# Kernel optimization log

Measured on AMD Instinct MI355X. Metric: run time of the kernel, lower is better.

The kernel has to match this reference:

```python
import jax, jax.numpy as jnp
import numpy as np

WEIGHT = 0.1
SELF_WEIGHT = 1.0
OTHER_WEIGHT = 1.0

def setup_inputs() -> dict:
    key = jax.random.key(0)
    k1, k2 = jax.random.split(key)
    B, D = 8192, 128
    output = jax.random.normal(k1, (B, D), dtype=jnp.float32)
    target = jax.random.normal(k2, (B, D), dtype=jnp.float32)
    return {"output": output, "target": target}

def reference(output, target):
    # Pairwise Euclidean distances d[i, n] = ||output[i] - target[n]||_2
    # no [B, B, D] intermediate).
    B = output.shape[0]
    xx = jnp.sum(output * output, axis=-1)          # [B]
    yy = jnp.sum(target * target, axis=-1)          # [B]
    d2 = xx[:, None] + yy[None, :] - 2.0 * (output @ target.T)  # [B, B]
    d = jnp.sqrt(jnp.maximum(d2, 0.0))
    diag_sum = jnp.trace(d)                          # sum of self distances
    total_sum = jnp.sum(d)
    other_sum = total_sum - diag_sum
    loss = (-diag_sum * SELF_WEIGHT + other_sum * OTHER_WEIGHT) / B * WEIGHT
    return loss
```

## Files before the change

kernel.cpp:

```cpp
#include <hip/hip_runtime.h>
#include <stdint.h>

typedef float f32x16 __attribute__((ext_vector_type(16)));
typedef int v8i __attribute__((ext_vector_type(8)));

#define BDIM 8192

__global__ __launch_bounds__(256) void prep_kernel(const float* __restrict__ out_f,
                                                   const float* __restrict__ tgt_f,
                                                   uint8_t* __restrict__ ak,
                                                   float* __restrict__ xxyy) {
    const float* src = blockIdx.y ? tgt_f : out_f;
    uint8_t* dst = ak + (size_t)blockIdx.y * (1u << 20);
    float* nrm = xxyy + (size_t)blockIdx.y * BDIM;

    const int tid = threadIdx.x;
    const int lane = tid & 63;
    const int w = tid >> 6;
    const int jg = lane & 15;
    const int r = blockIdx.x * 16 + w * 4 + (lane >> 4);

    const float4* s4 = (const float4*)(src + (size_t)r * 128 + jg * 8);
    float4 a = s4[0], b = s4[1];

    uint32_t w0 = __builtin_amdgcn_cvt_pk_fp8_f32(a.x, a.y, 0, false);
    w0 = __builtin_amdgcn_cvt_pk_fp8_f32(a.z, a.w, w0, true);
    uint32_t w1 = __builtin_amdgcn_cvt_pk_fp8_f32(b.x, b.y, 0, false);
    w1 = __builtin_amdgcn_cvt_pk_fp8_f32(b.z, b.w, w1, true);

    *(uint2*)(dst + (jg >> 3) * 524288 + ((jg >> 2) & 1) * 262144
                  + r * 32 + (jg & 3) * 8) = make_uint2(w0, w1);

    float sq = a.x*a.x + a.y*a.y + a.z*a.z + a.w*a.w
             + b.x*b.x + b.y*b.y + b.z*b.z + b.w*b.w;
    sq += __shfl_xor(sq, 1); sq += __shfl_xor(sq, 2);
    sq += __shfl_xor(sq, 4); sq += __shfl_xor(sq, 8);
    if (jg == 0) nrm[r] = sq;
}

__global__ __launch_bounds__(256, 4) void dist_kernel(const uint8_t* __restrict__ Ak,
                                                      const uint8_t* __restrict__ Bk,
                                                      const float* __restrict__ xxg,
                                                      const float* __restrict__ yyg,
                                                      float* __restrict__ partials) {
    __shared__ float xxl[128];
    __shared__ float yyl[128];
    __shared__ float wsum[4];

    const int tid = threadIdx.x;
    const int lane = tid & 63;
    const int wid = tid >> 6;
    const int wr = wid >> 1, wc = wid & 1;
    const int bx = blockIdx.x, by = blockIdx.y;

    if (tid < 128) xxl[tid] = xxg[bx * 128 + tid];
    else           yyl[tid - 128] = yyg[by * 128 + (tid - 128)];
    __syncthreads();

    const int lm = lane & 31;
    const int fh = lane >> 5;
    const uint8_t* pa = Ak + fh * 262144 + (size_t)(bx * 128 + wr * 64 + lm) * 32;
    const uint8_t* pb = Bk + fh * 262144 + (size_t)(by * 128 + wc * 64 + lm) * 32;

    f32x16 acc[2][2] = {};
    #pragma unroll
    for (int S = 0; S < 2; ++S) {
        v8i a0 = *(const v8i*)(pa + S * 524288);
        v8i a1 = *(const v8i*)(pa + S * 524288 + 1024);
        v8i b0 = *(const v8i*)(pb + S * 524288);
        v8i b1 = *(const v8i*)(pb + S * 524288 + 1024);
        acc[0][0] = __builtin_amdgcn_mfma_scale_f32_32x32x64_f8f6f4(
                        a0, b0, acc[0][0], 0, 0, 0, 0x7F7F7F7F, 0, 0x7F7F7F7F);
        acc[0][1] = __builtin_amdgcn_mfma_scale_f32_32x32x64_f8f6f4(
                        a0, b1, acc[0][1], 0, 0, 0, 0x7F7F7F7F, 0, 0x7F7F7F7F);
        acc[1][0] = __builtin_amdgcn_mfma_scale_f32_32x32x64_f8f6f4(
                        a1, b0, acc[1][0], 0, 0, 0, 0x7F7F7F7F, 0, 0x7F7F7F7F);
        acc[1][1] = __builtin_amdgcn_mfma_scale_f32_32x32x64_f8f6f4(
                        a1, b1, acc[1][1], 0, 0, 0, 0x7F7F7F7F, 0, 0x7F7F7F7F);
    }

    float s0 = 0.0f, s1 = 0.0f;
    #pragma unroll
    for (int tr = 0; tr < 2; ++tr) {
        float xv[16];
        #pragma unroll
        for (int r = 0; r < 16; ++r) {
            int ml = wr * 64 + tr * 32 + (r & 3) + 8 * (r >> 2) + 4 * fh;
            xv[r] = xxl[ml];
        }
        #pragma unroll
        for (int tc = 0; tc < 2; ++tc) {
            float yv = yyl[wc * 64 + tc * 32 + lm];
            #pragma unroll
            for (int r = 0; r < 16; ++r) {
                float d2 = fmaf(-2.0f, acc[tr][tc][r], xv[r] + yv);
                float d = __builtin_amdgcn_sqrtf(__builtin_fabsf(d2));
                if (r & 1) s1 += d; else s0 += d;
            }
        }
    }
    float s = s0 + s1;

    if (bx == by && wr == wc) {
        #pragma unroll
        for (int t = 0; t < 2; ++t) {
            #pragma unroll
            for (int r = 0; r < 16; ++r) {
                int row = (r & 3) + 8 * (r >> 2) + 4 * fh;
                if (row == lm) {
                    int idx = wr * 64 + t * 32 + row;
                    float d2 = fmaf(-2.0f, acc[t][t][r], xxl[idx] + yyl[idx]);
                    s -= 2.0f * __builtin_amdgcn_sqrtf(__builtin_fabsf(d2));
                }
            }
        }
    }

    #pragma unroll
    for (int off = 32; off > 0; off >>= 1) s += __shfl_down(s, off);
    if (lane == 0) wsum[wid] = s;
    __syncthreads();
    if (tid == 0) partials[by * 64 + bx] = wsum[0] + wsum[1] + wsum[2] + wsum[3];
}

__global__ __launch_bounds__(256) void reduce_kernel(const float* __restrict__ partials,
                                                     float* __restrict__ out) {
    __shared__ float wsum[4];
    float s = 0.0f;
    #pragma unroll
    for (int i = 0; i < 16; ++i) s += partials[threadIdx.x + i * 256];
    #pragma unroll
    for (int off = 32; off > 0; off >>= 1) s += __shfl_down(s, off);
    int lane = threadIdx.x & 63, wid = threadIdx.x >> 6;
    if (lane == 0) wsum[wid] = s;
    __syncthreads();
    if (threadIdx.x == 0)
        out[0] = (wsum[0] + wsum[1] + wsum[2] + wsum[3]) * (0.1f / 8192.0f);
}

extern "C" void kernel_launch(void* const* d_in, const int* in_sizes, int n_in,
                              void* d_out, int out_size, void* d_ws, size_t ws_size,
                              hipStream_t stream) {
    const float* output = (const float*)d_in[0];
    const float* target = (const float*)d_in[1];

    uint8_t* ws = (uint8_t*)d_ws;
    uint8_t* ak      = ws;
    float*   xxyy    = (float*)(ws + (2u << 20));
    float*   partial = (float*)(ws + (2u << 20) + (64u << 10));

    prep_kernel<<<dim3(512, 2), 256, 0, stream>>>(output, target, ak, xxyy);
    dist_kernel<<<dim3(64, 64), 256, 0, stream>>>(ak, ak + (1u << 20),
                                                  xxyy, xxyy + BDIM, partial);
    reduce_kernel<<<1, 256, 0, stream>>>(partial, (float*)d_out);
}
```

Measured before the change: 78.30 us.

## Stage FP8 tiles into LDS via direct global-to-LDS loads and fuse final reduction

The prep kernel now writes FP8 operands in a 16-byte-chunked layout. The distance kernel copies its A and B tiles into shared memory with global_load_lds, then reads the MFMA operands from LDS as two 16-byte halves instead of loading 32-byte vectors straight from global memory. The separate reduce kernel is removed and replaced by a last-block-done pattern that uses an atomic counter reset in prep, which saves one launch. The xx norm loads are also vectorized to float4. The cost is 32KB of LDS per block, which may limit occupancy, plus an atomic on every block.

```diff
diff --git a/kernel.cpp b/kernel.cpp
--- a/kernel.cpp
+++ b/kernel.cpp
@@ -3,13 +3,18 @@
 
 typedef float f32x16 __attribute__((ext_vector_type(16)));
 typedef int v8i __attribute__((ext_vector_type(8)));
+typedef int v4i __attribute__((ext_vector_type(4)));
 
 #define BDIM 8192
+
 
 __global__ __launch_bounds__(256) void prep_kernel(const float* __restrict__ out_f,
                                                    const float* __restrict__ tgt_f,
                                                    uint8_t* __restrict__ ak,
-                                                   float* __restrict__ xxyy) {
+                                                   float* __restrict__ xxyy,
+                                                   unsigned* __restrict__ cnt) {
+    if (blockIdx.x == 0 && blockIdx.y == 0 && threadIdx.x == 0) *cnt = 0u;
+
     const float* src = blockIdx.y ? tgt_f : out_f;
     uint8_t* dst = ak + (size_t)blockIdx.y * (1u << 20);
     float* nrm = xxyy + (size_t)blockIdx.y * BDIM;
@@ -29,7 +34,8 @@
     w1 = __builtin_amdgcn_cvt_pk_fp8_f32(b.z, b.w, w1, true);
 
     *(uint2*)(dst + (jg >> 3) * 524288 + ((jg >> 2) & 1) * 262144
-                  + r * 32 + (jg & 3) * 8) = make_uint2(w0, w1);
+                  + ((jg >> 1) & 1) * 131072 + r * 16 + (jg & 1) * 8)
+        = make_uint2(w0, w1);
 
     float sq = a.x*a.x + a.y*a.y + a.z*a.z + a.w*a.w
              + b.x*b.x + b.y*b.y + b.z*b.z + b.w*b.w;
@@ -42,10 +48,15 @@
                                                       const uint8_t* __restrict__ Bk,
                                                       const float* __restrict__ xxg,
                                                       const float* __restrict__ yyg,
-                                                      float* __restrict__ partials) {
+                                                      float* __restrict__ partials,
+                                                      unsigned* __restrict__ cnt,
+                                                      float* __restrict__ outp) {
+    __shared__ uint8_t sA[16384] __attribute__((aligned(16)));
+    __shared__ uint8_t sB[16384] __attribute__((aligned(16)));
     __shared__ float xxl[128];
     __shared__ float yyl[128];
     __shared__ float wsum[4];
+    __shared__ unsigned lastf;
 
     const int tid = threadIdx.x;
     const int lane = tid & 63;
@@ -53,22 +64,47 @@
     const int wr = wid >> 1, wc = wid & 1;
     const int bx = blockIdx.x, by = blockIdx.y;
 
+    {
+        const int c0 = wid * 8;
+        #pragma unroll
+        for (int i = 0; i < 8; ++i) {
+            int c = c0 + i;
+            int mat = c >> 4, rem = c & 15, s = rem >> 1, half = rem & 1;
+            int bidx = mat ? by : bx;
+            const uint8_t* g = (mat ? Bk : Ak)
+                + (s >> 2) * 524288 + ((s >> 1) & 1) * 262144 + (s & 1) * 131072
+                + ((size_t)(bidx * 128 + half * 64)) * 16 + lane * 16;
+            uint8_t* l = (mat ? sB : sA) + s * 2048 + half * 1024;
+            __builtin_amdgcn_global_load_lds(
+                (const __attribute__((address_space(1))) unsigned int*)g,
+                (__attribute__((address_space(3))) unsigned int*)l, 16, 0, 0);
+        }
+    }
     if (tid < 128) xxl[tid] = xxg[bx * 128 + tid];
     else           yyl[tid - 128] = yyg[by * 128 + (tid - 128)];
     __syncthreads();
 
     const int lm = lane & 31;
     const int fh = lane >> 5;
-    const uint8_t* pa = Ak + fh * 262144 + (size_t)(bx * 128 + wr * 64 + lm) * 32;
-    const uint8_t* pb = Bk + fh * 262144 + (size_t)(by * 128 + wc * 64 + lm) * 32;
+    const v4i* A4 = (const v4i*)sA;
+    const v4i* B4 = (const v4i*)sB;
 
     f32x16 acc[2][2] = {};
     #pragma unroll
     for (int S = 0; S < 2; ++S) {
-        v8i a0 = *(const v8i*)(pa + S * 524288);
-        v8i a1 = *(const v8i*)(pa + S * 524288 + 1024);
-        v8i b0 = *(const v8i*)(pb + S * 524288);
-        v8i b1 = *(const v8i*)(pb + S * 524288 + 1024);
+        const int sb = S * 4 + fh * 2;
+        v4i a0l = A4[(sb + 0) * 128 + wr * 64 + lm];
+        v4i a0h = A4[(sb + 1) * 128 + wr * 64 + lm];
+        v4i a1l = A4[(sb + 0) * 128 + wr * 64 + 32 + lm];
+        v4i a1h = A4[(sb + 1) * 128 + wr * 64 + 32 + lm];
+        v4i b0l = B4[(sb + 0) * 128 + wc * 64 + lm];
+        v4i b0h = B4[(sb + 1) * 128 + wc * 64 + lm];
+        v4i b1l = B4[(sb + 0) * 128 + wc * 64 + 32 + lm];
+        v4i b1h = B4[(sb + 1) * 128 + wc * 64 + 32 + lm];
+        v8i a0 = __builtin_shufflevector(a0l, a0h, 0, 1, 2, 3, 4, 5, 6, 7);
+        v8i a1 = __builtin_shufflevector(a1l, a1h, 0, 1, 2, 3, 4, 5, 6, 7);
+        v8i b0 = __builtin_shufflevector(b0l, b0h, 0, 1, 2, 3, 4, 5, 6, 7);
+        v8i b1 = __builtin_shufflevector(b1l, b1h, 0, 1, 2, 3, 4, 5, 6, 7);
         acc[0][0] = __builtin_amdgcn_mfma_scale_f32_32x32x64_f8f6f4(
                         a0, b0, acc[0][0], 0, 0, 0, 0x7F7F7F7F, 0, 0x7F7F7F7F);
         acc[0][1] = __builtin_amdgcn_mfma_scale_f32_32x32x64_f8f6f4(
@@ -84,9 +120,10 @@
     for (int tr = 0; tr < 2; ++tr) {
         float xv[16];
         #pragma unroll
-        for (int r = 0; r < 16; ++r) {
-            int ml = wr * 64 + tr * 32 + (r & 3) + 8 * (r >> 2) + 4 * fh;
-            xv[r] = xxl[ml];
+        for (int q = 0; q < 4; ++q) {
+            float4 t = *(const float4*)&xxl[wr * 64 + tr * 32 + 8 * q + 4 * fh];
+            xv[q * 4 + 0] = t.x; xv[q * 4 + 1] = t.y;
+            xv[q * 4 + 2] = t.z; xv[q * 4 + 3] = t.w;
         }
         #pragma unroll
         for (int tc = 0; tc < 2; ++tc) {
@@ -120,22 +157,30 @@
     for (int off = 32; off > 0; off >>= 1) s += __shfl_down(s, off);
     if (lane == 0) wsum[wid] = s;
     __syncthreads();
-    if (tid == 0) partials[by * 64 + bx] = wsum[0] + wsum[1] + wsum[2] + wsum[3];
-}
-
-__global__ __launch_bounds__(256) void reduce_kernel(const float* __restrict__ partials,
-                                                     float* __restrict__ out) {
-    __shared__ float wsum[4];
-    float s = 0.0f;
-    #pragma unroll
-    for (int i = 0; i < 16; ++i) s += partials[threadIdx.x + i * 256];
-    #pragma unroll
-    for (int off = 32; off > 0; off >>= 1) s += __shfl_down(s, off);
-    int lane = threadIdx.x & 63, wid = threadIdx.x >> 6;
-    if (lane == 0) wsum[wid] = s;
+
+    if (tid == 0) {
+        float bs = wsum[0] + wsum[1] + wsum[2] + wsum[3];
+        __hip_atomic_store(&partials[by * 64 + bx], bs,
+                           __ATOMIC_RELEASE, __HIP_MEMORY_SCOPE_AGENT);
+        unsigned old = __hip_atomic_fetch_add(cnt, 1u,
+                           __ATOMIC_ACQ_REL, __HIP_MEMORY_SCOPE_AGENT);
+        lastf = (old == 4095u) ? 1u : 0u;
+    }
     __syncthreads();
-    if (threadIdx.x == 0)
-        out[0] = (wsum[0] + wsum[1] + wsum[2] + wsum[3]) * (0.1f / 8192.0f);
+
+    if (lastf) {
+        float s2 = 0.0f;
+        #pragma unroll
+        for (int i = 0; i < 16; ++i)
+            s2 += __hip_atomic_load(&partials[tid + i * 256],
+                                    __ATOMIC_RELAXED, __HIP_MEMORY_SCOPE_AGENT);
+        #pragma unroll
+        for (int off = 32; off > 0; off >>= 1) s2 += __shfl_down(s2, off);
+        if (lane == 0) wsum[wid] = s2;
+        __syncthreads();
+        if (tid == 0)
+            outp[0] = (wsum[0] + wsum[1] + wsum[2] + wsum[3]) * (0.1f / 8192.0f);
+    }
 }
 
 extern "C" void kernel_launch(void* const* d_in, const int* in_sizes, int n_in,
@@ -145,12 +190,13 @@
     const float* target = (const float*)d_in[1];
 
     uint8_t* ws = (uint8_t*)d_ws;
-    uint8_t* ak      = ws;
-    float*   xxyy    = (float*)(ws + (2u << 20));
-    float*   partial = (float*)(ws + (2u << 20) + (64u << 10));
-
-    prep_kernel<<<dim3(512, 2), 256, 0, stream>>>(output, target, ak, xxyy);
+    uint8_t*  ak      = ws;
+    float*    xxyy    = (float*)(ws + (2u << 20));
+    float*    partial = (float*)(ws + (2u << 20) + (64u << 10));
+    unsigned* cnt     = (unsigned*)(ws + (2u << 20) + (80u << 10));
+
+    prep_kernel<<<dim3(512, 2), 256, 0, stream>>>(output, target, ak, xxyy, cnt);
     dist_kernel<<<dim3(64, 64), 256, 0, stream>>>(ak, ak + (1u << 20),
-                                                  xxyy, xxyy + BDIM, partial);
-    reduce_kernel<<<1, 256, 0, stream>>>(partial, (float*)d_out);
+                                                  xxyy, xxyy + BDIM, partial,
+                                                  cnt, (float*)d_out);
 }
```

After: 179.8 us. +129.6%, slower.

## Stage FP8 tiles through LDS via direct global-to-LDS loads

Applied to the files above, without the earlier changes.

Changes the prep kernel's FP8 layout to 16-byte row chunks and has the distance kernel load the block's A and B tiles into shared memory with global_load_lds. The MFMA operands are then read from LDS as two 16-byte vectors each, instead of each wave issuing 32-byte global loads for the same data. It also vectorises the xx norm reads into float4 LDS loads. The aim is to cut redundant global/L2 traffic and use wider coalesced loads, at the cost of 32KB LDS per block, which may limit occupancy.

```diff
diff --git a/kernel.cpp b/kernel.cpp
--- a/kernel.cpp
+++ b/kernel.cpp
@@ -3,8 +3,10 @@
 
 typedef float f32x16 __attribute__((ext_vector_type(16)));
 typedef int v8i __attribute__((ext_vector_type(8)));
+typedef int v4i __attribute__((ext_vector_type(4)));
 
 #define BDIM 8192
+
 
 __global__ __launch_bounds__(256) void prep_kernel(const float* __restrict__ out_f,
                                                    const float* __restrict__ tgt_f,
@@ -29,7 +31,8 @@
     w1 = __builtin_amdgcn_cvt_pk_fp8_f32(b.z, b.w, w1, true);
 
     *(uint2*)(dst + (jg >> 3) * 524288 + ((jg >> 2) & 1) * 262144
-                  + r * 32 + (jg & 3) * 8) = make_uint2(w0, w1);
+                  + ((jg >> 1) & 1) * 131072 + r * 16 + (jg & 1) * 8)
+        = make_uint2(w0, w1);
 
     float sq = a.x*a.x + a.y*a.y + a.z*a.z + a.w*a.w
              + b.x*b.x + b.y*b.y + b.z*b.z + b.w*b.w;
@@ -43,6 +46,8 @@
                                                       const float* __restrict__ xxg,
                                                       const float* __restrict__ yyg,
                                                       float* __restrict__ partials) {
+    __shared__ uint8_t sA[16384] __attribute__((aligned(16)));
+    __shared__ uint8_t sB[16384] __attribute__((aligned(16)));
     __shared__ float xxl[128];
     __shared__ float yyl[128];
     __shared__ float wsum[4];
@@ -53,22 +58,47 @@
     const int wr = wid >> 1, wc = wid & 1;
     const int bx = blockIdx.x, by = blockIdx.y;
 
+    {
+        const int c0 = wid * 8;
+        #pragma unroll
+        for (int i = 0; i < 8; ++i) {
+            int c = c0 + i;
+            int mat = c >> 4, rem = c & 15, s = rem >> 1, half = rem & 1;
+            int bidx = mat ? by : bx;
+            const uint8_t* g = (mat ? Bk : Ak)
+                + (s >> 2) * 524288 + ((s >> 1) & 1) * 262144 + (s & 1) * 131072
+                + ((size_t)(bidx * 128 + half * 64)) * 16 + lane * 16;
+            uint8_t* l = (mat ? sB : sA) + s * 2048 + half * 1024;
+            __builtin_amdgcn_global_load_lds(
+                (const __attribute__((address_space(1))) unsigned int*)g,
+                (__attribute__((address_space(3))) unsigned int*)l, 16, 0, 0);
+        }
+    }
     if (tid < 128) xxl[tid] = xxg[bx * 128 + tid];
     else           yyl[tid - 128] = yyg[by * 128 + (tid - 128)];
     __syncthreads();
 
     const int lm = lane & 31;
     const int fh = lane >> 5;
-    const uint8_t* pa = Ak + fh * 262144 + (size_t)(bx * 128 + wr * 64 + lm) * 32;
-    const uint8_t* pb = Bk + fh * 262144 + (size_t)(by * 128 + wc * 64 + lm) * 32;
+    const v4i* A4 = (const v4i*)sA;
+    const v4i* B4 = (const v4i*)sB;
 
     f32x16 acc[2][2] = {};
     #pragma unroll
     for (int S = 0; S < 2; ++S) {
-        v8i a0 = *(const v8i*)(pa + S * 524288);
-        v8i a1 = *(const v8i*)(pa + S * 524288 + 1024);
-        v8i b0 = *(const v8i*)(pb + S * 524288);
-        v8i b1 = *(const v8i*)(pb + S * 524288 + 1024);
+        const int sb = S * 4 + fh * 2;
+        v4i a0l = A4[(sb + 0) * 128 + wr * 64 + lm];
+        v4i a0h = A4[(sb + 1) * 128 + wr * 64 + lm];
+        v4i a1l = A4[(sb + 0) * 128 + wr * 64 + 32 + lm];
+        v4i a1h = A4[(sb + 1) * 128 + wr * 64 + 32 + lm];
+        v4i b0l = B4[(sb + 0) * 128 + wc * 64 + lm];
+        v4i b0h = B4[(sb + 1) * 128 + wc * 64 + lm];
+        v4i b1l = B4[(sb + 0) * 128 + wc * 64 + 32 + lm];
+        v4i b1h = B4[(sb + 1) * 128 + wc * 64 + 32 + lm];
+        v8i a0 = __builtin_shufflevector(a0l, a0h, 0, 1, 2, 3, 4, 5, 6, 7);
+        v8i a1 = __builtin_shufflevector(a1l, a1h, 0, 1, 2, 3, 4, 5, 6, 7);
+        v8i b0 = __builtin_shufflevector(b0l, b0h, 0, 1, 2, 3, 4, 5, 6, 7);
+        v8i b1 = __builtin_shufflevector(b1l, b1h, 0, 1, 2, 3, 4, 5, 6, 7);
         acc[0][0] = __builtin_amdgcn_mfma_scale_f32_32x32x64_f8f6f4(
                         a0, b0, acc[0][0], 0, 0, 0, 0x7F7F7F7F, 0, 0x7F7F7F7F);
         acc[0][1] = __builtin_amdgcn_mfma_scale_f32_32x32x64_f8f6f4(
@@ -84,9 +114,10 @@
     for (int tr = 0; tr < 2; ++tr) {
         float xv[16];
         #pragma unroll
-        for (int r = 0; r < 16; ++r) {
-            int ml = wr * 64 + tr * 32 + (r & 3) + 8 * (r >> 2) + 4 * fh;
-            xv[r] = xxl[ml];
+        for (int q = 0; q < 4; ++q) {
+            float4 t = *(const float4*)&xxl[wr * 64 + tr * 32 + 8 * q + 4 * fh];
+            xv[q * 4 + 0] = t.x; xv[q * 4 + 1] = t.y;
+            xv[q * 4 + 2] = t.z; xv[q * 4 + 3] = t.w;
         }
         #pragma unroll
         for (int tc = 0; tc < 2; ++tc) {
```

New measurement: 78.58 us, median of 2. About the same (+0.4%).
